# Kernel tuning notes

Measured on AMD Instinct MI355X. Metric: run time of the kernel, lower is better.

The kernel has to match this reference:

```python
import jax, jax.numpy as jnp
import numpy as np
import math

B, L, D = 4, 512, 768
H, DH, R = 12, 64, 128


def _layernorm(x, g, b, eps=1e-5):
    mu = jnp.mean(x, axis=-1, keepdims=True)
    var = jnp.var(x, axis=-1, keepdims=True)
    return (x - mu) * jax.lax.rsqrt(var + eps) * g + b


def setup_inputs() -> dict:
    key = jax.random.key(0)
    ks = jax.random.split(key, 8)
    s = 0.02
    return {
        "x": jax.random.normal(ks[0], (B, L, D), jnp.float32),
        "W_qkv": jax.random.normal(ks[1], (D, 3 * D), jnp.float32) * s,
        "b_qkv": jnp.zeros((3 * D,), jnp.float32),
        "W_b1": jax.random.normal(ks[2], (D, R), jnp.float32) * s,
        "W_b2": jax.random.normal(ks[3], (R, H * 5), jnp.float32) * s,
        "temperature": jnp.ones((1,), jnp.float32) * 0.5,
        "W_proj": jax.random.normal(ks[4], (D, D), jnp.float32) * s,
        "b_proj": jnp.zeros((D,), jnp.float32),
        "ln_g": jnp.ones((D,), jnp.float32),
        "ln_b": jnp.zeros((D,), jnp.float32),
        "mem_g": jnp.ones((DH,), jnp.float32),
        "mem_b": jnp.zeros((DH,), jnp.float32),
    }


def reference(x, W_qkv, b_qkv, W_b1, W_b2, temperature, W_proj, b_proj, ln_g, ln_b, mem_g, mem_b):
    Bq, Lq, Dq = x.shape
    xn = _layernorm(x, ln_g, ln_b)
    qkv = xn @ W_qkv + b_qkv
    q, k, v = jnp.split(qkv, 3, axis=-1)

    # bottleneck gating params: (B, L, H, 5)
    params = (jax.nn.silu(x @ W_b1) @ W_b2).reshape(Bq, Lq, H, 5)
    sem_amp = jax.nn.sigmoid(params[..., 0])
    sem_phase = jnp.tanh(params[..., 1]) * math.pi
    ctx_amp = jax.nn.sigmoid(params[..., 2])
    ctx_phase = jnp.tanh(params[..., 3]) * math.pi
    decay = 0.5 + 0.49 * jax.nn.sigmoid(params[..., 4])  # (B,L,H)

    temp = jnp.clip(temperature, 0.1, 2.0)  # (1,) broadcasts
    interference = jnp.tanh(sem_amp * ctx_amp * jnp.cos(sem_phase - ctx_phase)) * temp
    gate = jax.nn.sigmoid(interference)  # (B,L,H)

    qf = (jax.nn.elu(q) + 1.0).reshape(Bq, Lq, H, DH)
    kf = (jax.nn.elu(k) + 1.0).reshape(Bq, Lq, H, DH)
    vf = v.reshape(Bq, Lq, H, DH)

    log_decay = jnp.log(decay + 1e-8)
    cld = jnp.maximum(jnp.cumsum(log_decay, axis=1), -85.0)  # (B,L,H)
    df = jnp.exp(cld)
    inv_df = jnp.exp(-cld)
    ema = 1.0 - decay  # (B,L,H)

    # kv outer products gated by interference: (B,L,H,DH,DH)
    kv_all = jnp.einsum('blhd,blhe->blhde', kf, vf) * (1.0 + gate)[..., None, None]
    kv_states = jnp.cumsum(kv_all * (ema * inv_df)[..., None, None], axis=1) * df[..., None, None]

    z_states = jnp.cumsum(kf * (ema * inv_df)[..., None], axis=1) * df[..., None]  # (B,L,H,DH)

    out_num = jnp.einsum('blhd,blhde->blhe', qf, kv_states)
    den = jnp.sum(qf * z_states, axis=-1, keepdims=True) + 1e-6
    out = out_num / den  # (B,L,H,DH)

    out = _layernorm(out, mem_g, mem_b)
    attn_out = out.reshape(Bq, Lq, Dq)
    return attn_out @ W_proj + b_proj, gate
```

## Files before the change

kernel.cpp:

```cpp
#include <hip/hip_runtime.h>
#include <math.h>

#define PI_F 3.14159265358979323846f

static constexpr int L_ = 512, D_ = 768, H_ = 12, DH_ = 64;
static constexpr int BL_ = 2048;
static constexpr int BLD_ = BL_ * D_;
static constexpr int NC_ = 8;
static constexpr int BH_ = 48;

__global__ void sentinel_kernel(float* out, float code, float aux) {
  out[0] = code; out[1] = aux;
}

__global__ __launch_bounds__(256) void ln_stats(const float* __restrict__ x,
                                                float* __restrict__ murs) {
  int row = blockIdx.x, tid = threadIdx.x;
  const float* xr = x + (size_t)row * D_;
  float v0 = xr[tid], v1 = xr[tid + 256], v2 = xr[tid + 512];
  float s = v0 + v1 + v2;
  float s2 = v0 * v0 + v1 * v1 + v2 * v2;
#pragma unroll
  for (int off = 32; off > 0; off >>= 1) { s += __shfl_xor(s, off); s2 += __shfl_xor(s2, off); }
  __shared__ float red[8];
  if ((tid & 63) == 0) { red[tid >> 6] = s; red[4 + (tid >> 6)] = s2; }
  __syncthreads();
  if (tid == 0) {
    float st = red[0] + red[1] + red[2] + red[3];
    float qt = red[4] + red[5] + red[6] + red[7];
    float mu = st * (1.0f / D_);
    float var = qt * (1.0f / D_) - mu * mu;
    murs[2 * row] = mu;
    murs[2 * row + 1] = rsqrtf(var + 1e-5f);
  }
}

__global__ __launch_bounds__(128) void bottleneck_kernel(const float* __restrict__ x,
                                                         const float* __restrict__ Wb1,
                                                         const float* __restrict__ Wb2,
                                                         const float* __restrict__ temp_p,
                                                         float* __restrict__ gate_out,
                                                         float* __restrict__ cg,
                                                         float* __restrict__ ce,
                                                         float* __restrict__ ld) {
  int t = blockIdx.x;
  int tid = threadIdx.x;
  __shared__ float xs[768];
  __shared__ float hs[128];
  __shared__ float ps[60];
  const float* xr = x + (size_t)t * D_;
#pragma unroll
  for (int i = 0; i < 6; ++i) xs[tid + i * 128] = xr[tid + i * 128];
  __syncthreads();
  float acc = 0.f;
#pragma unroll 8
  for (int k = 0; k < 768; ++k) acc += xs[k] * Wb1[k * 128 + tid];
  hs[tid] = acc / (1.f + expf(-acc));
  __syncthreads();
  if (tid < 60) {
    float a = 0.f;
#pragma unroll 4
    for (int k = 0; k < 128; ++k) a += hs[k] * Wb2[k * 60 + tid];
    ps[tid] = a;
  }
  __syncthreads();
  if (tid < 12) {
    float p0 = ps[tid * 5 + 0], p1 = ps[tid * 5 + 1], p2 = ps[tid * 5 + 2];
    float p3 = ps[tid * 5 + 3], p4 = ps[tid * 5 + 4];
    float sa = 1.f / (1.f + expf(-p0));
    float sp = tanhf(p1) * PI_F;
    float ca = 1.f / (1.f + expf(-p2));
    float cp = tanhf(p3) * PI_F;
    float dec = 0.5f + 0.49f / (1.f + expf(-p4));
    float tmp = fminf(fmaxf(temp_p[0], 0.1f), 2.0f);
    float inter = tanhf(sa * ca * cosf(sp - cp)) * tmp;
    float gate = 1.f / (1.f + expf(-inter));
    gate_out[t * 12 + tid] = gate;
    int b = t >> 9, l = t & 511;
    int bhl = (b * 12 + tid) * L_ + l;
    float ema = 1.f - dec;
    cg[bhl] = ema * (1.f + gate);
    ce[bhl] = ema;
    ld[bhl] = logf(dec + 1e-8f);
  }
}

__global__ __launch_bounds__(256) void gemm_qkv(const float* __restrict__ x,
                                                const float* __restrict__ murs,
                                                const float* __restrict__ lg,
                                                const float* __restrict__ lb,
                                                const float* __restrict__ Bm,
                                                const float* __restrict__ bias,
                                                float* __restrict__ Oq,
                                                float* __restrict__ Ok,
                                                float* __restrict__ Ov) {
  const int N = 2304, K = 768;
  __shared__ float As[16][68];
  __shared__ float Bs[16][68];
  int tid = threadIdx.x;
  int tx = tid & 15, ty = tid >> 4;
  int row0 = blockIdx.y * 64, col0 = blockIdx.x * 64;
  float acc[4][4] = {};
  int ar = tid >> 2, ak = (tid & 3) * 4;
  int bk = tid >> 4, bc = (tid & 15) * 4;
  float2 m2 = *(const float2*)&murs[2 * (row0 + ar)];
  float mu = m2.x, rs = m2.y;
  const float* Arow = x + (size_t)(row0 + ar) * K;
  for (int k0 = 0; k0 < K; k0 += 16) {
    float4 a4 = *(const float4*)&Arow[k0 + ak];
    float4 g4 = *(const float4*)&lg[k0 + ak];
    float4 c4 = *(const float4*)&lb[k0 + ak];
    a4.x = (a4.x - mu) * rs * g4.x + c4.x;
    a4.y = (a4.y - mu) * rs * g4.y + c4.y;
    a4.z = (a4.z - mu) * rs * g4.z + c4.z;
    a4.w = (a4.w - mu) * rs * g4.w + c4.w;
    As[ak + 0][ar] = a4.x; As[ak + 1][ar] = a4.y;
    As[ak + 2][ar] = a4.z; As[ak + 3][ar] = a4.w;
    *(float4*)&Bs[bk][bc] = *(const float4*)&Bm[(size_t)(k0 + bk) * N + col0 + bc];
    __syncthreads();
#pragma unroll
    for (int kk = 0; kk < 16; ++kk) {
      float4 av = *(float4*)&As[kk][ty * 4];
      float4 bv = *(float4*)&Bs[kk][tx * 4];
      acc[0][0] += av.x * bv.x; acc[0][1] += av.x * bv.y; acc[0][2] += av.x * bv.z; acc[0][3] += av.x * bv.w;
      acc[1][0] += av.y * bv.x; acc[1][1] += av.y * bv.y; acc[1][2] += av.y * bv.z; acc[1][3] += av.y * bv.w;
      acc[2][0] += av.z * bv.x; acc[2][1] += av.z * bv.y; acc[2][2] += av.z * bv.z; acc[2][3] += av.z * bv.w;
      acc[3][0] += av.w * bv.x; acc[3][1] += av.w * bv.y; acc[3][2] += av.w * bv.z; acc[3][3] += av.w * bv.w;
    }
    __syncthreads();
  }
  int sec = col0 / 768;
  float* O = (sec == 0) ? Oq : ((sec == 1) ? Ok : Ov);
  int lc = col0 - sec * 768 + tx * 4;
  float b0 = bias[col0 + tx * 4 + 0], b1 = bias[col0 + tx * 4 + 1];
  float b2 = bias[col0 + tx * 4 + 2], b3 = bias[col0 + tx * 4 + 3];
#pragma unroll
  for (int ii = 0; ii < 4; ++ii) {
    int r = row0 + ty * 4 + ii;
    float4 v;
    v.x = acc[ii][0] + b0; v.y = acc[ii][1] + b1;
    v.z = acc[ii][2] + b2; v.w = acc[ii][3] + b3;
    if (sec < 2) {
      v.x = (v.x > 0.f) ? v.x + 1.f : expf(v.x);
      v.y = (v.y > 0.f) ? v.y + 1.f : expf(v.y);
      v.z = (v.z > 0.f) ? v.z + 1.f : expf(v.z);
      v.w = (v.w > 0.f) ? v.w + 1.f : expf(v.w);
    }
    *(float4*)&O[(size_t)r * 768 + lc] = v;
  }
}

__global__ __launch_bounds__(256) void gemm_proj(const float* __restrict__ A,
                                                 const float* __restrict__ Bm,
                                                 const float* __restrict__ bias,
                                                 float* __restrict__ O0,
                                                 int N, int K) {
  __shared__ float As[16][68];
  __shared__ float Bs[16][68];
  int tid = threadIdx.x;
  int tx = tid & 15, ty = tid >> 4;
  int row0 = blockIdx.y * 64, col0 = blockIdx.x * 64;
  float acc[4][4] = {};
  int ar = tid >> 2, ak = (tid & 3) * 4;
  int bk = tid >> 4, bc = (tid & 15) * 4;
  for (int k0 = 0; k0 < K; k0 += 16) {
    float4 a4 = *(const float4*)&A[(size_t)(row0 + ar) * K + k0 + ak];
    As[ak + 0][ar] = a4.x; As[ak + 1][ar] = a4.y;
    As[ak + 2][ar] = a4.z; As[ak + 3][ar] = a4.w;
    *(float4*)&Bs[bk][bc] = *(const float4*)&Bm[(size_t)(k0 + bk) * N + col0 + bc];
    __syncthreads();
#pragma unroll
    for (int kk = 0; kk < 16; ++kk) {
      float4 av = *(float4*)&As[kk][ty * 4];
      float4 bv = *(float4*)&Bs[kk][tx * 4];
      acc[0][0] += av.x * bv.x; acc[0][1] += av.x * bv.y; acc[0][2] += av.x * bv.z; acc[0][3] += av.x * bv.w;
      acc[1][0] += av.y * bv.x; acc[1][1] += av.y * bv.y; acc[1][2] += av.y * bv.z; acc[1][3] += av.y * bv.w;
      acc[2][0] += av.z * bv.x; acc[2][1] += av.z * bv.y; acc[2][2] += av.z * bv.z; acc[2][3] += av.z * bv.w;
      acc[3][0] += av.w * bv.x; acc[3][1] += av.w * bv.y; acc[3][2] += av.w * bv.z; acc[3][3] += av.w * bv.w;
    }
    __syncthreads();
  }
  float b0 = bias[col0 + tx * 4 + 0], b1 = bias[col0 + tx * 4 + 1];
  float b2 = bias[col0 + tx * 4 + 2], b3 = bias[col0 + tx * 4 + 3];
#pragma unroll
  for (int ii = 0; ii < 4; ++ii) {
    int r = row0 + ty * 4 + ii;
    float4 v;
    v.x = acc[ii][0] + b0; v.y = acc[ii][1] + b1;
    v.z = acc[ii][2] + b2; v.w = acc[ii][3] + b3;
    *(float4*)&O0[(size_t)r * N + col0 + tx * 4] = v;
  }
}

__global__ __launch_bounds__(64) void cld_kernel(const float* __restrict__ ld,
                                                 float* __restrict__ cld,
                                                 float* __restrict__ cEnd) {
  int bh = blockIdx.x;
  int lane = threadIdx.x;
  const float* src = ld + (size_t)bh * L_;
  float v[8];
  float s = 0.f;
#pragma unroll
  for (int i = 0; i < 8; ++i) { v[i] = src[lane * 8 + i]; s += v[i]; }
  float tot = s;
#pragma unroll
  for (int off = 1; off < 64; off <<= 1) {
    float n = __shfl_up(tot, off);
    if (lane >= off) tot += n;
  }
  float run = tot - s;
  float out7 = 0.f;
#pragma unroll
  for (int i = 0; i < 8; ++i) {
    run += v[i];
    float o = fmaxf(run, -85.f);
    cld[(size_t)bh * L_ + lane * 8 + i] = o;
    out7 = o;
  }
  if ((lane & 7) == 7) cEnd[bh * NC_ + (lane >> 3)] = out7;
}

__global__ __launch_bounds__(64) void infscan_kernel(const float* __restrict__ kf,
                                                     const float* __restrict__ ce,
                                                     const float* __restrict__ cld,
                                                     int* __restrict__ tstar) {
  int bh = blockIdx.x;
  int b = bh / H_, h = bh - b * H_;
  int e = threadIdx.x;
  float cz = 0.f;
  int tf = L_;
  for (int t = 0; t < L_; ++t) {
    int idx = bh * L_ + t;
    float s = ce[idx] * expf(-cld[idx]);
    float kv = kf[(size_t)(b * L_ + t) * D_ + h * DH_ + e];
    cz = cz + kv * s;
    if (tf == L_ && isinf(cz)) tf = t;
  }
#pragma unroll
  for (int off = 1; off < 64; off <<= 1) tf = min(tf, __shfl_xor(tf, off));
  if (e == 0) tstar[bh] = tf;
}

__global__ __launch_bounds__(256) void chunk_sum_kernel(const float* __restrict__ kf,
                                                        const float* __restrict__ vf,
                                                        const float* __restrict__ cg,
                                                        const float* __restrict__ ce,
                                                        const float* __restrict__ cld,
                                                        const float* __restrict__ cEnd,
                                                        float* __restrict__ T,
                                                        float* __restrict__ zc) {
  int blk = blockIdx.x;
  int c = blk & 7, bh = blk >> 3;
  int b = bh / H_, h = bh - b * H_;
  int tid = threadIdx.x;
  __shared__ float kfs[64][68];
  __shared__ float vfs[64][68];
  __shared__ float wv[64], wz[64];
  float cend = cEnd[blk];
  if (tid < 64) {
    int idx = bh * L_ + c * 64 + tid;
    float w = expf(cend - cld[idx]);
    wv[tid] = cg[idx] * w;
    wz[tid] = ce[idx] * w;
  }
  __syncthreads();
  int t = tid >> 2, g4 = (tid & 3) * 16;
  size_t rowb = (size_t)(b * L_ + c * 64 + t) * D_ + h * 64 + g4;
  float wvt = wv[t];
#pragma unroll
  for (int i = 0; i < 4; ++i) {
    *(float4*)&kfs[t][g4 + 4 * i] = *(const float4*)&kf[rowb + 4 * i];
    float4 vv = *(const float4*)&vf[rowb + 4 * i];
    vv.x *= wvt; vv.y *= wvt; vv.z *= wvt; vv.w *= wvt;
    *(float4*)&vfs[t][g4 + 4 * i] = vv;
  }
  __syncthreads();
  int d = tid >> 2, eb = (tid & 3) * 16;
  float4 a0 = {}, a1 = {}, a2 = {}, a3 = {};
  for (int tt = 0; tt < 64; ++tt) {
    float kd = kfs[tt][d];
    float4 x0 = *(float4*)&vfs[tt][eb + 0];
    float4 x1 = *(float4*)&vfs[tt][eb + 4];
    float4 x2 = *(float4*)&vfs[tt][eb + 8];
    float4 x3 = *(float4*)&vfs[tt][eb + 12];
    a0.x += kd * x0.x; a0.y += kd * x0.y; a0.z += kd * x0.z; a0.w += kd * x0.w;
    a1.x += kd * x1.x; a1.y += kd * x1.y; a1.z += kd * x1.z; a1.w += kd * x1.w;
    a2.x += kd * x2.x; a2.y += kd * x2.y; a2.z += kd * x2.z; a2.w += kd * x2.w;
    a3.x += kd * x3.x; a3.y += kd * x3.y; a3.z += kd * x3.z; a3.w += kd * x3.w;
  }
  size_t tb = (size_t)blk * 4096 + (size_t)d * 64 + eb;
  *(float4*)&T[tb + 0] = a0;
  *(float4*)&T[tb + 4] = a1;
  *(float4*)&T[tb + 8] = a2;
  *(float4*)&T[tb + 12] = a3;
  if (tid < 64) {
    float za = 0.f;
#pragma unroll 8
    for (int tt = 0; tt < 64; ++tt) za += kfs[tt][tid] * wz[tt];
    zc[blk * 64 + tid] = za;
  }
}

__global__ __launch_bounds__(256) void scan_kernel(float* __restrict__ T,
                                                   const float* __restrict__ zc,
                                                   const float* __restrict__ cEnd,
                                                   float* __restrict__ zprev) {
  int bh = blockIdx.x, tid = threadIdx.x;
  float4 s0 = {}, s1 = {}, s2 = {}, s3 = {};
  float zs = 0.f;
  float prevEnd = 0.f;
  for (int c = 0; c < NC_; ++c) {
    int blk = bh * NC_ + c;
    float r = expf(cEnd[blk] - prevEnd);
    prevEnd = cEnd[blk];
    size_t base = (size_t)blk * 4096 + (size_t)tid * 16;
    float4 t0 = *(const float4*)&T[base + 0];
    float4 t1 = *(const float4*)&T[base + 4];
    float4 t2 = *(const float4*)&T[base + 8];
    float4 t3 = *(const float4*)&T[base + 12];
    *(float4*)&T[base + 0] = s0;
    *(float4*)&T[base + 4] = s1;
    *(float4*)&T[base + 8] = s2;
    *(float4*)&T[base + 12] = s3;
    s0.x = s0.x * r + t0.x; s0.y = s0.y * r + t0.y; s0.z = s0.z * r + t0.z; s0.w = s0.w * r + t0.w;
    s1.x = s1.x * r + t1.x; s1.y = s1.y * r + t1.y; s1.z = s1.z * r + t1.z; s1.w = s1.w * r + t1.w;
    s2.x = s2.x * r + t2.x; s2.y = s2.y * r + t2.y; s2.z = s2.z * r + t2.z; s2.w = s2.w * r + t2.w;
    s3.x = s3.x * r + t3.x; s3.y = s3.y * r + t3.y; s3.z = s3.z * r + t3.z; s3.w = s3.w * r + t3.w;
    if (tid < 64) {
      zprev[blk * 64 + tid] = zs;
      zs = zs * r + zc[blk * 64 + tid];
    }
  }
}

__global__ __launch_bounds__(256) void chunk_out_kernel(const float* __restrict__ qf,
                                                        const float* __restrict__ kf,
                                                        const float* __restrict__ vf,
                                                        const float* __restrict__ cg,
                                                        const float* __restrict__ ce,
                                                        const float* __restrict__ cld,
                                                        const float* __restrict__ cEnd,
                                                        const float* __restrict__ Sprev,
                                                        const float* __restrict__ zprev,
                                                        const int* __restrict__ tstar,
                                                        const float* __restrict__ mg,
                                                        const float* __restrict__ mb,
                                                        float* __restrict__ attn) {
  int blk = blockIdx.x;
  int c = blk & 7, bh = blk >> 3;
  int b = bh / H_, h = bh - b * H_;
  int tid = threadIdx.x;
  __shared__ float qfs[64][68];
  __shared__ float kfs[64][68];
  __shared__ float vfs[64][68];
  __shared__ float cldS[64], cgS[64], ceS[64], zS[64];
  int t = tid >> 2, g4 = (tid & 3) * 16;
  size_t rowb = (size_t)(b * L_ + c * 64 + t) * D_ + h * 64 + g4;
#pragma unroll
  for (int i = 0; i < 4; ++i) {
    *(float4*)&qfs[t][g4 + 4 * i] = *(const float4*)&qf[rowb + 4 * i];
    *(float4*)&kfs[t][g4 + 4 * i] = *(const float4*)&kf[rowb + 4 * i];
    *(float4*)&vfs[t][g4 + 4 * i] = *(const float4*)&vf[rowb + 4 * i];
  }
  if (tid < 64) {
    int idx = bh * L_ + c * 64 + tid;
    cldS[tid] = cld[idx];
    cgS[tid] = cg[idx];
    ceS[tid] = ce[idx];
    zS[tid] = zprev[blk * 64 + tid];
  }
  __syncthreads();
  float prevEnd = (c == 0) ? 0.f : cEnd[blk - 1];
  int ts = tstar[bh];
  int i = tid >> 2, jb = (tid & 3) * 16;
  float sc[16];
#pragma unroll
  for (int jj = 0; jj < 16; ++jj) sc[jj] = 0.f;
  for (int d = 0; d < 64; d += 4) {
    float4 q4 = *(float4*)&qfs[i][d];
#pragma unroll
    for (int jj = 0; jj < 16; ++jj) {
      float4 k4 = *(float4*)&kfs[jb + jj][d];
      sc[jj] += q4.x * k4.x + q4.y * k4.y + q4.z * k4.z + q4.w * k4.w;
    }
  }
  float cldi = cldS[i];
  float den = 0.f;
  float mvals[16];
#pragma unroll
  for (int jj = 0; jj < 16; ++jj) {
    int j = jb + jj;
    float w = (j <= i) ? expf(cldi - cldS[j]) : 0.f;
    float sw = sc[jj] * w;
    den += sw * ceS[j];
    mvals[jj] = sw * cgS[j];
  }
  float dz = 0.f;
#pragma unroll
  for (int dd = 0; dd < 16; ++dd) dz += qfs[i][jb + dd] * zS[jb + dd];
  den += __shfl_xor(den, 1); den += __shfl_xor(den, 2);
  dz += __shfl_xor(dz, 1);  dz += __shfl_xor(dz, 2);
  float wi = expf(cldi - prevEnd);
  den += wi * dz + 1e-6f;
  __syncthreads();
#pragma unroll
  for (int jj = 0; jj < 16; ++jj) kfs[i][jb + jj] = mvals[jj];
  __syncthreads();
  float4 o0 = {}, o1 = {}, o2 = {}, o3 = {};
  for (int j = 0; j < 64; ++j) {
    float m = kfs[i][j];
    float4 x0 = *(float4*)&vfs[j][jb + 0];
    float4 x1 = *(float4*)&vfs[j][jb + 4];
    float4 x2 = *(float4*)&vfs[j][jb + 8];
    float4 x3 = *(float4*)&vfs[j][jb + 12];
    o0.x += m * x0.x; o0.y += m * x0.y; o0.z += m * x0.z; o0.w += m * x0.w;
    o1.x += m * x1.x; o1.y += m * x1.y; o1.z += m * x1.z; o1.w += m * x1.w;
    o2.x += m * x2.x; o2.y += m * x2.y; o2.z += m * x2.z; o2.w += m * x2.w;
    o3.x += m * x3.x; o3.y += m * x3.y; o3.z += m * x3.z; o3.w += m * x3.w;
  }
  float4 p0 = {}, p1 = {}, p2 = {}, p3 = {};
  size_t sb = (size_t)blk * 4096;
  for (int d = 0; d < 64; ++d) {
    float qd = qfs[i][d];
    float4 x0 = *(const float4*)&Sprev[sb + d * 64 + jb + 0];
    float4 x1 = *(const float4*)&Sprev[sb + d * 64 + jb + 4];
    float4 x2 = *(const float4*)&Sprev[sb + d * 64 + jb + 8];
    float4 x3 = *(const float4*)&Sprev[sb + d * 64 + jb + 12];
    p0.x += qd * x0.x; p0.y += qd * x0.y; p0.z += qd * x0.z; p0.w += qd * x0.w;
    p1.x += qd * x1.x; p1.y += qd * x1.y; p1.z += qd * x1.z; p1.w += qd * x1.w;
    p2.x += qd * x2.x; p2.y += qd * x2.y; p2.z += qd * x2.z; p2.w += qd * x2.w;
    p3.x += qd * x3.x; p3.y += qd * x3.y; p3.z += qd * x3.z; p3.w += qd * x3.w;
  }
  size_t ob = (size_t)(b * L_ + c * 64 + i) * D_ + h * 64 + jb;
  if (c * 64 + i >= ts) {
#pragma unroll
    for (int q4i = 0; q4i < 4; ++q4i) {
      float4 w4;
      w4.x = mb[jb + q4i * 4 + 0]; w4.y = mb[jb + q4i * 4 + 1];
      w4.z = mb[jb + q4i * 4 + 2]; w4.w = mb[jb + q4i * 4 + 3];
      *(float4*)&attn[ob + q4i * 4] = w4;
    }
    return;
  }
  float inv = 1.0f / den;
  float o[16];
  o[0] = (o0.x + wi * p0.x) * inv;  o[1] = (o0.y + wi * p0.y) * inv;
  o[2] = (o0.z + wi * p0.z) * inv;  o[3] = (o0.w + wi * p0.w) * inv;
  o[4] = (o1.x + wi * p1.x) * inv;  o[5] = (o1.y + wi * p1.y) * inv;
  o[6] = (o1.z + wi * p1.z) * inv;  o[7] = (o1.w + wi * p1.w) * inv;
  o[8] = (o2.x + wi * p2.x) * inv;  o[9] = (o2.y + wi * p2.y) * inv;
  o[10] = (o2.z + wi * p2.z) * inv; o[11] = (o2.w + wi * p2.w) * inv;
  o[12] = (o3.x + wi * p3.x) * inv; o[13] = (o3.y + wi * p3.y) * inv;
  o[14] = (o3.z + wi * p3.z) * inv; o[15] = (o3.w + wi * p3.w) * inv;
  float s = 0.f, s2 = 0.f;
#pragma unroll
  for (int e2 = 0; e2 < 16; ++e2) { s += o[e2]; s2 += o[e2] * o[e2]; }
  s += __shfl_xor(s, 1);  s += __shfl_xor(s, 2);
  s2 += __shfl_xor(s2, 1); s2 += __shfl_xor(s2, 2);
  float mu = s * (1.f / 64.f);
  float var = s2 * (1.f / 64.f) - mu * mu;
  float rs = rsqrtf(var + 1e-5f);
#pragma unroll
  for (int q4i = 0; q4i < 4; ++q4i) {
    float4 w4;
    w4.x = (o[q4i * 4 + 0] - mu) * rs * mg[jb + q4i * 4 + 0] + mb[jb + q4i * 4 + 0];
    w4.y = (o[q4i * 4 + 1] - mu) * rs * mg[jb + q4i * 4 + 1] + mb[jb + q4i * 4 + 1];
    w4.z = (o[q4i * 4 + 2] - mu) * rs * mg[jb + q4i * 4 + 2] + mb[jb + q4i * 4 + 2];
    w4.w = (o[q4i * 4 + 3] - mu) * rs * mg[jb + q4i * 4 + 3] + mb[jb + q4i * 4 + 3];
    *(float4*)&attn[ob + q4i * 4] = w4;
  }
}

extern "C" void kernel_launch(void* const* d_in, const int* in_sizes, int n_in,
                              void* d_out, int out_size, void* d_ws, size_t ws_size,
                              hipStream_t stream) {
  const float* x     = (const float*)d_in[0];
  const float* Wqkv  = (const float*)d_in[1];
  const float* bqkv  = (const float*)d_in[2];
  const float* Wb1   = (const float*)d_in[3];
  const float* Wb2   = (const float*)d_in[4];
  const float* temp  = (const float*)d_in[5];
  const float* Wproj = (const float*)d_in[6];
  const float* bproj = (const float*)d_in[7];
  const float* lng   = (const float*)d_in[8];
  const float* lnb   = (const float*)d_in[9];
  const float* memg  = (const float*)d_in[10];
  const float* memb  = (const float*)d_in[11];
  float* out0 = (float*)d_out;
  float* gate = out0 + BLD_;

  static const int expect[12] = {1572864, 1769472, 2304, 98304, 7680, 1,
                                 589824, 768, 768, 768, 64, 64};
  int bad = (n_in == 12) ? -1 : 99;
  if (bad < 0) for (int i = 0; i < 12; ++i) if (in_sizes[i] != expect[i]) { bad = i; break; }
  size_t need = (size_t)(4 * BLD_ + 262144 + 4 * 24576) * sizeof(float);
  if (bad >= 0) { sentinel_kernel<<<1, 1, 0, stream>>>(out0, 3.0e6f, (float)bad); return; }
  if (ws_size < need) { sentinel_kernel<<<1, 1, 0, stream>>>(out0, 1.0e6f, (float)(ws_size >> 20)); return; }

  float* ws   = (float*)d_ws;
  float* xn   = ws;
  float* qfb  = xn + BLD_;
  float* kfb  = qfb + BLD_;
  float* vfb  = kfb + BLD_;
  float* h1   = vfb + BLD_;
  float* cgb  = h1 + 262144;
  float* ceb  = cgb + 24576;
  float* ldb  = ceb + 24576;
  float* cldb = ldb + 24576;
  float* murs = xn;
  float* Tb   = xn;
  float* zcb  = h1;
  float* zpv  = h1 + 24576;
  float* cEnd = h1 + 49152;
  int*   tstar = (int*)(h1 + 49536);
  float* attn = qfb;

  ln_stats<<<BL_, 256, 0, stream>>>(x, murs);
  bottleneck_kernel<<<BL_, 128, 0, stream>>>(x, Wb1, Wb2, temp, gate, cgb, ceb, ldb);
  cld_kernel<<<BH_, 64, 0, stream>>>(ldb, cldb, cEnd);
  gemm_qkv<<<dim3(36, 32), 256, 0, stream>>>(x, murs, lng, lnb, Wqkv, bqkv, qfb, kfb, vfb);
  infscan_kernel<<<BH_, 64, 0, stream>>>(kfb, ceb, cldb, tstar);
  chunk_sum_kernel<<<BH_ * NC_, 256, 0, stream>>>(kfb, vfb, cgb, ceb, cldb, cEnd, Tb, zcb);
  scan_kernel<<<BH_, 256, 0, stream>>>(Tb, zcb, cEnd, zpv);
  chunk_out_kernel<<<BH_ * NC_, 256, 0, stream>>>(qfb, kfb, vfb, cgb, ceb, cldb, cEnd,
                                                  Tb, zpv, tstar, memg, memb, attn);
  gemm_proj<<<dim3(12, 32), 256, 0, stream>>>(attn, Wproj, bproj, out0, 768, 768);
}
```

Measured before the change: 416.4 us.

## Register-prefetch GEMM tiles with K-step 32 and fuse cld scan into infscan

Both the QKV and projection GEMMs now use a 32-deep K tile. The next tile's global loads (including the fused layernorm) are prefetched into registers while the current tile is computed from shared memory, which hides global latency and halves the number of barriers. Separately, the cumulative log-decay scan is merged with the overflow-detection scan into one kernel. That kernel keeps the per-timestep scale factors in shared memory, removing a launch and repeated exp and global reads. The trade-offs are more shared memory and registers per GEMM block, and the serial infscan loop still dominates its kernel.

```diff
diff --git a/kernel.cpp b/kernel.cpp
--- a/kernel.cpp
+++ b/kernel.cpp
@@ -95,8 +95,8 @@
                                                 float* __restrict__ Ok,
                                                 float* __restrict__ Ov) {
   const int N = 2304, K = 768;
-  __shared__ float As[16][68];
-  __shared__ float Bs[16][68];
+  __shared__ float As[32][68];
+  __shared__ float Bs[32][68];
   int tid = threadIdx.x;
   int tx = tid & 15, ty = tid >> 4;
   int row0 = blockIdx.y * 64, col0 = blockIdx.x * 64;
@@ -106,20 +106,42 @@
   float2 m2 = *(const float2*)&murs[2 * (row0 + ar)];
   float mu = m2.x, rs = m2.y;
   const float* Arow = x + (size_t)(row0 + ar) * K;
-  for (int k0 = 0; k0 < K; k0 += 16) {
-    float4 a4 = *(const float4*)&Arow[k0 + ak];
-    float4 g4 = *(const float4*)&lg[k0 + ak];
-    float4 c4 = *(const float4*)&lb[k0 + ak];
-    a4.x = (a4.x - mu) * rs * g4.x + c4.x;
-    a4.y = (a4.y - mu) * rs * g4.y + c4.y;
-    a4.z = (a4.z - mu) * rs * g4.z + c4.z;
-    a4.w = (a4.w - mu) * rs * g4.w + c4.w;
-    As[ak + 0][ar] = a4.x; As[ak + 1][ar] = a4.y;
-    As[ak + 2][ar] = a4.z; As[ak + 3][ar] = a4.w;
-    *(float4*)&Bs[bk][bc] = *(const float4*)&Bm[(size_t)(k0 + bk) * N + col0 + bc];
+  float4 a0, a1, b0, b1;
+  {
+    float4 r0 = *(const float4*)&Arow[ak];
+    float4 r1 = *(const float4*)&Arow[16 + ak];
+    float4 g0 = *(const float4*)&lg[ak],      c0 = *(const float4*)&lb[ak];
+    float4 g1 = *(const float4*)&lg[16 + ak], c1 = *(const float4*)&lb[16 + ak];
+    a0.x = (r0.x - mu) * rs * g0.x + c0.x; a0.y = (r0.y - mu) * rs * g0.y + c0.y;
+    a0.z = (r0.z - mu) * rs * g0.z + c0.z; a0.w = (r0.w - mu) * rs * g0.w + c0.w;
+    a1.x = (r1.x - mu) * rs * g1.x + c1.x; a1.y = (r1.y - mu) * rs * g1.y + c1.y;
+    a1.z = (r1.z - mu) * rs * g1.z + c1.z; a1.w = (r1.w - mu) * rs * g1.w + c1.w;
+    b0 = *(const float4*)&Bm[(size_t)bk * N + col0 + bc];
+    b1 = *(const float4*)&Bm[(size_t)(16 + bk) * N + col0 + bc];
+  }
+  for (int k0 = 0; k0 < K; k0 += 32) {
+    As[ak + 0][ar] = a0.x; As[ak + 1][ar] = a0.y;
+    As[ak + 2][ar] = a0.z; As[ak + 3][ar] = a0.w;
+    As[16 + ak + 0][ar] = a1.x; As[16 + ak + 1][ar] = a1.y;
+    As[16 + ak + 2][ar] = a1.z; As[16 + ak + 3][ar] = a1.w;
+    *(float4*)&Bs[bk][bc] = b0;
+    *(float4*)&Bs[16 + bk][bc] = b1;
     __syncthreads();
-#pragma unroll
-    for (int kk = 0; kk < 16; ++kk) {
+    if (k0 + 32 < K) {
+      int kn = k0 + 32;
+      float4 r0 = *(const float4*)&Arow[kn + ak];
+      float4 r1 = *(const float4*)&Arow[kn + 16 + ak];
+      float4 g0 = *(const float4*)&lg[kn + ak],      c0 = *(const float4*)&lb[kn + ak];
+      float4 g1 = *(const float4*)&lg[kn + 16 + ak], c1 = *(const float4*)&lb[kn + 16 + ak];
+      a0.x = (r0.x - mu) * rs * g0.x + c0.x; a0.y = (r0.y - mu) * rs * g0.y + c0.y;
+      a0.z = (r0.z - mu) * rs * g0.z + c0.z; a0.w = (r0.w - mu) * rs * g0.w + c0.w;
+      a1.x = (r1.x - mu) * rs * g1.x + c1.x; a1.y = (r1.y - mu) * rs * g1.y + c1.y;
+      a1.z = (r1.z - mu) * rs * g1.z + c1.z; a1.w = (r1.w - mu) * rs * g1.w + c1.w;
+      b0 = *(const float4*)&Bm[(size_t)(kn + bk) * N + col0 + bc];
+      b1 = *(const float4*)&Bm[(size_t)(kn + 16 + bk) * N + col0 + bc];
+    }
+#pragma unroll
+    for (int kk = 0; kk < 32; ++kk) {
       float4 av = *(float4*)&As[kk][ty * 4];
       float4 bv = *(float4*)&Bs[kk][tx * 4];
       acc[0][0] += av.x * bv.x; acc[0][1] += av.x * bv.y; acc[0][2] += av.x * bv.z; acc[0][3] += av.x * bv.w;
@@ -132,14 +154,14 @@
   int sec = col0 / 768;
   float* O = (sec == 0) ? Oq : ((sec == 1) ? Ok : Ov);
   int lc = col0 - sec * 768 + tx * 4;
-  float b0 = bias[col0 + tx * 4 + 0], b1 = bias[col0 + tx * 4 + 1];
-  float b2 = bias[col0 + tx * 4 + 2], b3 = bias[col0 + tx * 4 + 3];
+  float b0s = bias[col0 + tx * 4 + 0], b1s = bias[col0 + tx * 4 + 1];
+  float b2s = bias[col0 + tx * 4 + 2], b3s = bias[col0 + tx * 4 + 3];
 #pragma unroll
   for (int ii = 0; ii < 4; ++ii) {
     int r = row0 + ty * 4 + ii;
     float4 v;
-    v.x = acc[ii][0] + b0; v.y = acc[ii][1] + b1;
-    v.z = acc[ii][2] + b2; v.w = acc[ii][3] + b3;
+    v.x = acc[ii][0] + b0s; v.y = acc[ii][1] + b1s;
+    v.z = acc[ii][2] + b2s; v.w = acc[ii][3] + b3s;
     if (sec < 2) {
       v.x = (v.x > 0.f) ? v.x + 1.f : expf(v.x);
       v.y = (v.y > 0.f) ? v.y + 1.f : expf(v.y);
@@ -155,22 +177,37 @@
                                                  const float* __restrict__ bias,
                                                  float* __restrict__ O0,
                                                  int N, int K) {
-  __shared__ float As[16][68];
-  __shared__ float Bs[16][68];
+  __shared__ float As[32][68];
+  __shared__ float Bs[32][68];
   int tid = threadIdx.x;
   int tx = tid & 15, ty = tid >> 4;
   int row0 = blockIdx.y * 64, col0 = blockIdx.x * 64;
   float acc[4][4] = {};
   int ar = tid >> 2, ak = (tid & 3) * 4;
   int bk = tid >> 4, bc = (tid & 15) * 4;
-  for (int k0 = 0; k0 < K; k0 += 16) {
-    float4 a4 = *(const float4*)&A[(size_t)(row0 + ar) * K + k0 + ak];
-    As[ak + 0][ar] = a4.x; As[ak + 1][ar] = a4.y;
-    As[ak + 2][ar] = a4.z; As[ak + 3][ar] = a4.w;
-    *(float4*)&Bs[bk][bc] = *(const float4*)&Bm[(size_t)(k0 + bk) * N + col0 + bc];
+  const float* Arow = A + (size_t)ar * K + (size_t)row0 * K;
+  float4 a0, a1, b0, b1;
+  a0 = *(const float4*)&Arow[ak];
+  a1 = *(const float4*)&Arow[16 + ak];
+  b0 = *(const float4*)&Bm[(size_t)bk * N + col0 + bc];
+  b1 = *(const float4*)&Bm[(size_t)(16 + bk) * N + col0 + bc];
+  for (int k0 = 0; k0 < K; k0 += 32) {
+    As[ak + 0][ar] = a0.x; As[ak + 1][ar] = a0.y;
+    As[ak + 2][ar] = a0.z; As[ak + 3][ar] = a0.w;
+    As[16 + ak + 0][ar] = a1.x; As[16 + ak + 1][ar] = a1.y;
+    As[16 + ak + 2][ar] = a1.z; As[16 + ak + 3][ar] = a1.w;
+    *(float4*)&Bs[bk][bc] = b0;
+    *(float4*)&Bs[16 + bk][bc] = b1;
     __syncthreads();
-#pragma unroll
-    for (int kk = 0; kk < 16; ++kk) {
+    if (k0 + 32 < K) {
+      int kn = k0 + 32;
+      a0 = *(const float4*)&Arow[kn + ak];
+      a1 = *(const float4*)&Arow[kn + 16 + ak];
+      b0 = *(const float4*)&Bm[(size_t)(kn + bk) * N + col0 + bc];
+      b1 = *(const float4*)&Bm[(size_t)(kn + 16 + bk) * N + col0 + bc];
+    }
+#pragma unroll
+    for (int kk = 0; kk < 32; ++kk) {
       float4 av = *(float4*)&As[kk][ty * 4];
       float4 bv = *(float4*)&Bs[kk][tx * 4];
       acc[0][0] += av.x * bv.x; acc[0][1] += av.x * bv.y; acc[0][2] += av.x * bv.z; acc[0][3] += av.x * bv.w;
@@ -180,23 +217,28 @@
     }
     __syncthreads();
   }
-  float b0 = bias[col0 + tx * 4 + 0], b1 = bias[col0 + tx * 4 + 1];
-  float b2 = bias[col0 + tx * 4 + 2], b3 = bias[col0 + tx * 4 + 3];
+  float b0s = bias[col0 + tx * 4 + 0], b1s = bias[col0 + tx * 4 + 1];
+  float b2s = bias[col0 + tx * 4 + 2], b3s = bias[col0 + tx * 4 + 3];
 #pragma unroll
   for (int ii = 0; ii < 4; ++ii) {
     int r = row0 + ty * 4 + ii;
     float4 v;
-    v.x = acc[ii][0] + b0; v.y = acc[ii][1] + b1;
-    v.z = acc[ii][2] + b2; v.w = acc[ii][3] + b3;
+    v.x = acc[ii][0] + b0s; v.y = acc[ii][1] + b1s;
+    v.z = acc[ii][2] + b2s; v.w = acc[ii][3] + b3s;
     *(float4*)&O0[(size_t)r * N + col0 + tx * 4] = v;
   }
 }
 
-__global__ __launch_bounds__(64) void cld_kernel(const float* __restrict__ ld,
-                                                 float* __restrict__ cld,
-                                                 float* __restrict__ cEnd) {
+__global__ __launch_bounds__(64) void cldinf_kernel(const float* __restrict__ ld,
+                                                    const float* __restrict__ ce,
+                                                    const float* __restrict__ kf,
+                                                    float* __restrict__ cld,
+                                                    float* __restrict__ cEnd,
+                                                    int* __restrict__ tstar) {
   int bh = blockIdx.x;
+  int b = bh / H_, h = bh - b * H_;
   int lane = threadIdx.x;
+  __shared__ float sArr[512];
   const float* src = ld + (size_t)bh * L_;
   float v[8];
   float s = 0.f;
@@ -214,31 +256,24 @@
   for (int i = 0; i < 8; ++i) {
     run += v[i];
     float o = fmaxf(run, -85.f);
-    cld[(size_t)bh * L_ + lane * 8 + i] = o;
+    int idx = bh * L_ + lane * 8 + i;
+    cld[idx] = o;
+    sArr[lane * 8 + i] = ce[idx] * expf(-o);
     out7 = o;
   }
   if ((lane & 7) == 7) cEnd[bh * NC_ + (lane >> 3)] = out7;
-}
-
-__global__ __launch_bounds__(64) void infscan_kernel(const float* __restrict__ kf,
-                                                     const float* __restrict__ ce,
-                                                     const float* __restrict__ cld,
-                                                     int* __restrict__ tstar) {
-  int bh = blockIdx.x;
-  int b = bh / H_, h = bh - b * H_;
-  int e = threadIdx.x;
+  __syncthreads();
   float cz = 0.f;
   int tf = L_;
+  const float* kcol = kf + (size_t)(b * L_) * D_ + h * DH_ + lane;
   for (int t = 0; t < L_; ++t) {
-    int idx = bh * L_ + t;
-    float s = ce[idx] * expf(-cld[idx]);
-    float kv = kf[(size_t)(b * L_ + t) * D_ + h * DH_ + e];
-    cz = cz + kv * s;
+    float kv = kcol[(size_t)t * D_];
+    cz = cz + kv * sArr[t];
     if (tf == L_ && isinf(cz)) tf = t;
   }
 #pragma unroll
   for (int off = 1; off < 64; off <<= 1) tf = min(tf, __shfl_xor(tf, off));
-  if (e == 0) tstar[bh] = tf;
+  if (lane == 0) tstar[bh] = tf;
 }
 
 __global__ __launch_bounds__(256) void chunk_sum_kernel(const float* __restrict__ kf,
@@ -517,9 +552,8 @@
 
   ln_stats<<<BL_, 256, 0, stream>>>(x, murs);
   bottleneck_kernel<<<BL_, 128, 0, stream>>>(x, Wb1, Wb2, temp, gate, cgb, ceb, ldb);
-  cld_kernel<<<BH_, 64, 0, stream>>>(ldb, cldb, cEnd);
   gemm_qkv<<<dim3(36, 32), 256, 0, stream>>>(x, murs, lng, lnb, Wqkv, bqkv, qfb, kfb, vfb);
-  infscan_kernel<<<BH_, 64, 0, stream>>>(kfb, ceb, cldb, tstar);
+  cldinf_kernel<<<BH_, 64, 0, stream>>>(ldb, ceb, kfb, cldb, cEnd, tstar);
   chunk_sum_kernel<<<BH_ * NC_, 256, 0, stream>>>(kfb, vfb, cgb, ceb, cldb, cEnd, Tb, zcb);
   scan_kernel<<<BH_, 256, 0, stream>>>(Tb, zcb, cEnd, zpv);
   chunk_out_kernel<<<BH_ * NC_, 256, 0, stream>>>(qfb, kfb, vfb, cgb, ceb, cldb, cEnd,
```

Result: faster. 399.5 us (-4.0%).
